# Kernel tuning notes

Measured on AMD Instinct MI355X. Metric: run time of the kernel, lower is better.

The kernel has to match this reference:

```python
import jax, jax.numpy as jnp
import numpy as np


def _quaternion_F(R):
    """Build the batched 4x4 quaternion key matrix F from R: (B,3,3) -> (B,4,4).
    Largest eigenvalue of F gives the optimal rotational overlap (Theobald 2005)."""
    r00, r01, r02 = R[:, 0, 0], R[:, 0, 1], R[:, 0, 2]
    r10, r11, r12 = R[:, 1, 0], R[:, 1, 1], R[:, 1, 2]
    r20, r21, r22 = R[:, 2, 0], R[:, 2, 1], R[:, 2, 2]
    row0 = jnp.stack([r00 + r11 + r22, r12 - r21, r20 - r02, r01 - r10], axis=-1)
    row1 = jnp.stack([r12 - r21, r00 - r11 - r22, r01 + r10, r02 + r20], axis=-1)
    row2 = jnp.stack([r20 - r02, r01 + r10, -r00 + r11 - r22, r12 + r21], axis=-1)
    row3 = jnp.stack([r01 - r10, r02 + r20, r12 + r21, -r00 - r11 + r22], axis=-1)
    return jnp.stack([row0, row1, row2, row3], axis=-2)  # (B,4,4)


def setup_inputs() -> dict:
    key = jax.random.key(0)
    k1, k2 = jax.random.split(key)
    B, N = 4096, 2048
    y_prime = jax.random.normal(k1, (B, N, 3), dtype=jnp.float32)
    y = jax.random.normal(k2, (B, N, 3), dtype=jnp.float32)
    return {"y_prime": y_prime, "y": y}


def reference(y_prime, y):
    # NOTE: original module computes translated copies but uses the
    # UNTRANSLATED tensors in the batch loop; we faithfully reproduce that.
    n_atoms = y_prime.shape[1]
    # Per-sample cross-covariance R = y_prime[i].T @ y[i], batched: (B,3,3)
    R = jnp.einsum('bnd,bne->bde', y_prime, y)
    F = _quaternion_F(R)                       # (B,4,4) symmetric
    vals = jnp.linalg.eigh(F)[0]               # ascending eigenvalues, (B,4)
    lam_max = vals[:, -1]                      # (B,)
    sq_norms = jnp.sum(y_prime * y_prime, axis=(1, 2)) + jnp.sum(y * y, axis=(1, 2))
    sd = sq_norms - 2.0 * lam_max              # per-sample squared deviation
    total_sd = jnp.sum(sd)
    return jnp.sqrt(total_sd / n_atoms)
```

## Files before the change

kernel.cpp:

```cpp
#include <hip/hip_runtime.h>
#include <math.h>

#define THREADS 256
#define N_ATOMS 2048

__global__ __launch_bounds__(THREADS) void rmsd_batch_kernel(
    const float* __restrict__ yp, const float* __restrict__ yy,
    double* __restrict__ sd)
{
    const int b = blockIdx.x;
    const int t = threadIdx.x;
    const float4* A  = reinterpret_cast<const float4*>(yp + (size_t)b * (N_ATOMS * 3));
    const float4* Bv = reinterpret_cast<const float4*>(yy + (size_t)b * (N_ATOMS * 3));

    float sxx = 0.f, sxy = 0.f, sxz = 0.f;
    float syx = 0.f, syy = 0.f, syz = 0.f;
    float szx = 0.f, szy = 0.f, szz = 0.f;
    float na = 0.f, nb = 0.f;

    #pragma unroll
    for (int it = 0; it < 2; ++it) {
        const int g = t + it * THREADS;
        const float4 a0 = A[3 * g + 0];
        const float4 a1 = A[3 * g + 1];
        const float4 a2 = A[3 * g + 2];
        const float4 b0 = Bv[3 * g + 0];
        const float4 b1 = Bv[3 * g + 1];
        const float4 b2 = Bv[3 * g + 2];

        float px[4], py[4], pz[4], qx[4], qy[4], qz[4];
        px[0] = a0.x; py[0] = a0.y; pz[0] = a0.z;
        px[1] = a0.w; py[1] = a1.x; pz[1] = a1.y;
        px[2] = a1.z; py[2] = a1.w; pz[2] = a2.x;
        px[3] = a2.y; py[3] = a2.z; pz[3] = a2.w;
        qx[0] = b0.x; qy[0] = b0.y; qz[0] = b0.z;
        qx[1] = b0.w; qy[1] = b1.x; qz[1] = b1.y;
        qx[2] = b1.z; qy[2] = b1.w; qz[2] = b2.x;
        qx[3] = b2.y; qy[3] = b2.z; qz[3] = b2.w;

        #pragma unroll
        for (int k = 0; k < 4; ++k) {
            sxx += px[k] * qx[k]; sxy += px[k] * qy[k]; sxz += px[k] * qz[k];
            syx += py[k] * qx[k]; syy += py[k] * qy[k]; syz += py[k] * qz[k];
            szx += pz[k] * qx[k]; szy += pz[k] * qy[k]; szz += pz[k] * qz[k];
            na  += px[k] * px[k] + py[k] * py[k] + pz[k] * pz[k];
            nb  += qx[k] * qx[k] + qy[k] * qy[k] + qz[k] * qz[k];
        }
    }

    float vals[11] = {sxx, sxy, sxz, syx, syy, syz, szx, szy, szz, na, nb};
    #pragma unroll
    for (int k = 0; k < 11; ++k) {
        #pragma unroll
        for (int off = 32; off > 0; off >>= 1)
            vals[k] += __shfl_down(vals[k], off, 64);
    }

    __shared__ float red[4][11];
    const int wave = t >> 6, lane = t & 63;
    if (lane == 0) {
        #pragma unroll
        for (int k = 0; k < 11; ++k) red[wave][k] = vals[k];
    }
    __syncthreads();

    if (t == 0) {
        double S[11];
        #pragma unroll
        for (int k = 0; k < 11; ++k)
            S[k] = (double)red[0][k] + (double)red[1][k] +
                   (double)red[2][k] + (double)red[3][k];
        const double Sxx = S[0], Sxy = S[1], Sxz = S[2];
        const double Syx = S[3], Syy = S[4], Syz = S[5];
        const double Szx = S[6], Szy = S[7], Szz = S[8];
        const double sqn = S[9] + S[10];

        const double Sxx2 = Sxx * Sxx, Syy2 = Syy * Syy, Szz2 = Szz * Szz;
        const double Sxy2 = Sxy * Sxy, Syz2 = Syz * Syz, Sxz2 = Sxz * Sxz;
        const double Syx2 = Syx * Syx, Szy2 = Szy * Szy, Szx2 = Szx * Szx;

        const double SyzSzymSyySzz2 = 2.0 * (Syz * Szy - Syy * Szz);
        const double Sxx2Syy2Szz2Syz2Szy2 = Syy2 + Szz2 - Sxx2 + Syz2 + Szy2;

        const double C2 = -2.0 * (Sxx2 + Syy2 + Szz2 + Sxy2 + Syx2 + Sxz2 + Szx2 + Syz2 + Szy2);
        const double C1 = 8.0 * (Sxx * Syz * Szy + Syy * Szx * Sxz + Szz * Sxy * Syx -
                                 Sxx * Syy * Szz - Syz * Szx * Sxy - Szy * Syx * Sxz);

        const double SxzpSzx = Sxz + Szx;
        const double SyzpSzy = Syz + Szy;
        const double SxypSyx = Sxy + Syx;
        const double SyzmSzy = Syz - Szy;
        const double SxzmSzx = Sxz - Szx;
        const double SxymSyx = Sxy - Syx;
        const double SxxpSyy = Sxx + Syy;
        const double SxxmSyy = Sxx - Syy;
        const double Sxy2Sxz2Syx2Szx2 = Sxy2 + Sxz2 - Syx2 - Szx2;

        const double C0 =
            Sxy2Sxz2Syx2Szx2 * Sxy2Sxz2Syx2Szx2
            + (Sxx2Syy2Szz2Syz2Szy2 + SyzSzymSyySzz2) * (Sxx2Syy2Szz2Syz2Szy2 - SyzSzymSyySzz2)
            + (-(SxzpSzx) * (SyzmSzy) + (SxymSyx) * (SxxmSyy - Szz)) *
              (-(SxzmSzx) * (SyzpSzy) + (SxymSyx) * (SxxmSyy + Szz))
            + (-(SxzpSzx) * (SyzpSzy) - (SxypSyx) * (SxxpSyy - Szz)) *
              (-(SxzmSzx) * (SyzmSzy) - (SxypSyx) * (SxxpSyy + Szz))
            + (+(SxypSyx) * (SyzpSzy) + (SxzpSzx) * (SxxmSyy + Szz)) *
              (-(SxymSyx) * (SyzmSzy) + (SxzpSzx) * (SxxpSyy + Szz))
            + (+(SxypSyx) * (SyzmSzy) + (SxzmSzx) * (SxxmSyy - Szz)) *
              (-(SxymSyx) * (SyzpSzy) + (SxzmSzx) * (SxxpSyy - Szz));

        double lam = 0.5 * sqn;
        for (int i = 0; i < 100; ++i) {
            const double old = lam;
            const double x2 = lam * lam;
            const double bp = (x2 + C2) * lam;
            const double ap = bp + C1;
            const double den = 2.0 * x2 * lam + bp + ap;
            if (den == 0.0) break;
            lam -= (ap * lam + C0) / den;
            if (fabs(lam - old) < fabs(1e-13 * lam)) break;
        }
        sd[b] = sqn - 2.0 * lam;
    }
}

__global__ __launch_bounds__(256) void rmsd_final_kernel(
    const double* __restrict__ sd, int Bn, float* __restrict__ out)
{
    const int t = threadIdx.x;
    double s = 0.0;
    for (int i = t; i < Bn; i += 256) s += sd[i];
    #pragma unroll
    for (int off = 32; off > 0; off >>= 1)
        s += __shfl_down(s, off, 64);
    __shared__ double red[4];
    if ((t & 63) == 0) red[t >> 6] = s;
    __syncthreads();
    if (t == 0) {
        const double tot = red[0] + red[1] + red[2] + red[3];
        out[0] = (float)sqrt(tot / (double)N_ATOMS);
    }
}

extern "C" void kernel_launch(void* const* d_in, const int* in_sizes, int n_in,
                              void* d_out, int out_size, void* d_ws, size_t ws_size,
                              hipStream_t stream) {
    const float* yp = (const float*)d_in[0];
    const float* yy = (const float*)d_in[1];
    float* out = (float*)d_out;
    const int B = in_sizes[0] / (N_ATOMS * 3);

    double* sd = (double*)d_ws;

    rmsd_batch_kernel<<<B, THREADS, 0, stream>>>(yp, yy, sd);
    rmsd_final_kernel<<<1, 256, 0, stream>>>(sd, B, out);
}
```

Baseline: 42.90 us.

## Map one wavefront per batch sample and move eigen solve into final reduction

Each wavefront now handles a whole sample, so the block-level shared-memory reduction and barrier go away, and the per-sample 11 sums are written to a workspace. The serial double-precision Newton solve, which used to run on thread 0 of every block, moves into a single 1024-thread kernel that does the eigenvalue solve and the final sum together. This shortens the streaming kernel's tail. The cost is about 4096 double-precision Newton solves spread over only 1024 threads in one workgroup, which may become a serial bottleneck.

```diff
diff --git a/kernel.cpp b/kernel.cpp
--- a/kernel.cpp
+++ b/kernel.cpp
@@ -1,15 +1,16 @@
 #include <hip/hip_runtime.h>
 #include <math.h>
 
-#define THREADS 256
 #define N_ATOMS 2048
 
-__global__ __launch_bounds__(THREADS) void rmsd_batch_kernel(
+__global__ __launch_bounds__(256) void rmsd_partial_kernel(
     const float* __restrict__ yp, const float* __restrict__ yy,
-    double* __restrict__ sd)
+    float* __restrict__ part )
 {
-    const int b = blockIdx.x;
-    const int t = threadIdx.x;
+    const int wave = threadIdx.x >> 6;
+    const int lane = threadIdx.x & 63;
+    const int b = blockIdx.x * 4 + wave;
+
     const float4* A  = reinterpret_cast<const float4*>(yp + (size_t)b * (N_ATOMS * 3));
     const float4* Bv = reinterpret_cast<const float4*>(yy + (size_t)b * (N_ATOMS * 3));
 
@@ -18,9 +19,9 @@
     float szx = 0.f, szy = 0.f, szz = 0.f;
     float na = 0.f, nb = 0.f;
 
-    #pragma unroll
-    for (int it = 0; it < 2; ++it) {
-        const int g = t + it * THREADS;
+    #pragma unroll 2
+    for (int it = 0; it < 8; ++it) {
+        const int g = lane + it * 64;
         const float4 a0 = A[3 * g + 0];
         const float4 a1 = A[3 * g + 1];
         const float4 a2 = A[3 * g + 2];
@@ -56,24 +57,25 @@
             vals[k] += __shfl_down(vals[k], off, 64);
     }
 
-    __shared__ float red[4][11];
-    const int wave = t >> 6, lane = t & 63;
     if (lane == 0) {
+        float* dst = part + (size_t)b * 11;
         #pragma unroll
-        for (int k = 0; k < 11; ++k) red[wave][k] = vals[k];
+        for (int k = 0; k < 11; ++k) dst[k] = vals[k];
     }
-    __syncthreads();
+}
 
-    if (t == 0) {
-        double S[11];
-        #pragma unroll
-        for (int k = 0; k < 11; ++k)
-            S[k] = (double)red[0][k] + (double)red[1][k] +
-                   (double)red[2][k] + (double)red[3][k];
+__global__ __launch_bounds__(1024) void rmsd_eigen_reduce_kernel(
+    const float* __restrict__ part, int Bn, float* __restrict__ out)
+{
+    const int t = threadIdx.x;
+    double acc = 0.0;
+
+    for (int b = t; b < Bn; b += 1024) {
+        const float* S = part + (size_t)b * 11;
         const double Sxx = S[0], Sxy = S[1], Sxz = S[2];
         const double Syx = S[3], Syy = S[4], Syz = S[5];
         const double Szx = S[6], Szy = S[7], Szz = S[8];
-        const double sqn = S[9] + S[10];
+        const double sqn = (double)S[9] + (double)S[10];
 
         const double Sxx2 = Sxx * Sxx, Syy2 = Syy * Syy, Szz2 = Szz * Szz;
         const double Sxy2 = Sxy * Sxy, Syz2 = Syz * Syz, Sxz2 = Sxz * Sxz;
@@ -119,24 +121,21 @@
             lam -= (ap * lam + C0) / den;
             if (fabs(lam - old) < fabs(1e-13 * lam)) break;
         }
-        sd[b] = sqn - 2.0 * lam;
+        acc += sqn - 2.0 * lam;
     }
-}
 
-__global__ __launch_bounds__(256) void rmsd_final_kernel(
-    const double* __restrict__ sd, int Bn, float* __restrict__ out)
-{
-    const int t = threadIdx.x;
-    double s = 0.0;
-    for (int i = t; i < Bn; i += 256) s += sd[i];
     #pragma unroll
     for (int off = 32; off > 0; off >>= 1)
-        s += __shfl_down(s, off, 64);
-    __shared__ double red[4];
-    if ((t & 63) == 0) red[t >> 6] = s;
+        acc += __shfl_down(acc, off, 64);
+
+    __shared__ double red[16];
+    if ((t & 63) == 0) red[t >> 6] = acc;
     __syncthreads();
+
     if (t == 0) {
-        const double tot = red[0] + red[1] + red[2] + red[3];
+        double tot = 0.0;
+        #pragma unroll
+        for (int i = 0; i < 16; ++i) tot += red[i];
         out[0] = (float)sqrt(tot / (double)N_ATOMS);
     }
 }
@@ -149,8 +148,8 @@
     float* out = (float*)d_out;
     const int B = in_sizes[0] / (N_ATOMS * 3);
 
-    double* sd = (double*)d_ws;
+    float* part = (float*)d_ws;
 
-    rmsd_batch_kernel<<<B, THREADS, 0, stream>>>(yp, yy, sd);
-    rmsd_final_kernel<<<1, 256, 0, stream>>>(sd, B, out);
+    rmsd_partial_kernel<<<B / 4, 256, 0, stream>>>(yp, yy, part);
+    rmsd_eigen_reduce_kernel<<<1, 1024, 0, stream>>>(part, B, out);
 }
```

Measured after the change: 61.78 us. +44.0%, slower.
